# Kernel tuning notes

Hardware: AMD Instinct MI355X
Metric: run time of the kernel (lower is better)

## Reference

```python
import jax, jax.numpy as jnp
import numpy as np

B, T, C, H, M = 2, 2048, 1024, 16, 64
EPS = 1e-5


def _ln(x, g, b):
    mu = jnp.mean(x, axis=-1, keepdims=True)
    var = jnp.mean(jnp.square(x - mu), axis=-1, keepdims=True)
    return (x - mu) * jax.lax.rsqrt(var + EPS) * g + b


def setup_inputs() -> dict:
    key = jax.random.key(0)
    ks = jax.random.split(key, 16)
    s = lambda fan_in: 1.0 / np.sqrt(fan_in)
    return {
        'x': jax.random.normal(ks[0], (B, T, C), jnp.float32),
        'ln1_g': jnp.ones((C,), jnp.float32),
        'ln1_b': jnp.zeros((C,), jnp.float32),
        'attn_w': jax.random.normal(ks[1], (C, 3 * C), jnp.float32) * s(C),
        'attn_b': jnp.zeros((3 * C,), jnp.float32),
        'proj_w': jax.random.normal(ks[2], (C, C), jnp.float32) * s(C),
        'proj_b': jnp.zeros((C,), jnp.float32),
        'a1_dw': jax.random.normal(ks[3], (C, M), jnp.float32) * s(C),
        'a1_db': jnp.zeros((M,), jnp.float32),
        'a1_uw': jax.random.normal(ks[4], (M, C), jnp.float32) * s(M),
        'a1_ub': jnp.zeros((C,), jnp.float32),
        'ln2_g': jnp.ones((C,), jnp.float32),
        'ln2_b': jnp.zeros((C,), jnp.float32),
        'fc_w': jax.random.normal(ks[5], (C, 4 * C), jnp.float32) * s(C),
        'fc_b': jnp.zeros((4 * C,), jnp.float32),
        'mlp_pw': jax.random.normal(ks[6], (4 * C, C), jnp.float32) * s(4 * C),
        'mlp_pb': jnp.zeros((C,), jnp.float32),
        'a2_dw': jax.random.normal(ks[7], (C, M), jnp.float32) * s(C),
        'a2_db': jnp.zeros((M,), jnp.float32),
        'a2_uw': jax.random.normal(ks[8], (M, C), jnp.float32) * s(M),
        'a2_ub': jnp.zeros((C,), jnp.float32),
    }


def _attn(x, attn_w, attn_b, proj_w, proj_b):
    b, t, c = x.shape
    hd = c // H
    qkv = x @ attn_w + attn_b                      # [B,T,3C]
    q, k, v = jnp.split(qkv, 3, axis=-1)
    q = q.reshape(b, t, H, hd).transpose(0, 2, 1, 3)  # [B,H,T,hd]
    k = k.reshape(b, t, H, hd).transpose(0, 2, 1, 3)
    v = v.reshape(b, t, H, hd).transpose(0, 2, 1, 3)
    att = jnp.einsum('bhqd,bhkd->bhqk', q, k) * (1.0 / np.sqrt(hd))
    mask = jnp.tril(jnp.ones((t, t), bool))
    att = jnp.where(mask, att, -jnp.inf)
    att = jax.nn.softmax(att, axis=-1)
    y = jnp.einsum('bhqk,bhkd->bhqd', att, v)      # [B,H,T,hd]
    y = y.transpose(0, 2, 1, 3).reshape(b, t, c)
    return y @ proj_w + proj_b


def _adapter(x, dw, db, uw, ub):
    return jax.nn.relu(x @ dw + db) @ uw + ub


def reference(x, ln1_g, ln1_b, attn_w, attn_b, proj_w, proj_b,
              a1_dw, a1_db, a1_uw, a1_ub, ln2_g, ln2_b,
              fc_w, fc_b, mlp_pw, mlp_pb, a2_dw, a2_db, a2_uw, a2_ub):
    x = x + _attn(_ln(x, ln1_g, ln1_b), attn_w, attn_b, proj_w, proj_b)
    x = x + _adapter(x, a1_dw, a1_db, a1_uw, a1_ub)
    h = _ln(x, ln2_g, ln2_b)
    h = jax.nn.gelu(h @ fc_w + fc_b, approximate=True) @ mlp_pw + mlp_pb
    x = x + h
    x = x + _adapter(x, a2_dw, a2_db, a2_uw, a2_ub)
    return x
```

## Files before the change

kernel.cpp:

```cpp
#include <hip/hip_runtime.h>
#include <hip/hip_bf16.h>
#include <cstdint>

#define DEVI __device__ __forceinline__

using bf16x8 = __attribute__((ext_vector_type(8))) short;
using f32x4  = __attribute__((ext_vector_type(4))) float;

DEVI short f2b(float f) {
  __hip_bfloat16 h = __float2bfloat16(f);
  return *reinterpret_cast<short*>(&h);
}
DEVI float b2f(short s) {
  __hip_bfloat16 h = *reinterpret_cast<__hip_bfloat16*>(&s);
  return __bfloat162float(h);
}
DEVI uint32_t pk2(float a, float b) {
  return (uint32_t)(uint16_t)f2b(a) | ((uint32_t)(uint16_t)f2b(b) << 16);
}

DEVI f32x4 mfma16(bf16x8 a, bf16x8 b, f32x4 c) {
  return __builtin_amdgcn_mfma_f32_16x16x32_bf16(a, b, c, 0, 0, 0);
}

DEVI void gload_lds16(const void* g, void* l) {
  __builtin_amdgcn_global_load_lds(
      (const __attribute__((address_space(1))) void*)g,
      (__attribute__((address_space(3))) void*)l, 16, 0, 0);
}

DEVI float gelu_f(float x) {
  float u = 1.5957691216057308f * (x + 0.044715f * x * x * x);
  float e = __expf(u);
  float t = 1.f - 2.f / (e + 1.f);
  return 0.5f * x * (1.f + t);
}

__global__ void k_wt(const float* __restrict__ in, short* __restrict__ out,
                     int R, int Cc) {
  __shared__ float tile[32][33];
  int c0 = blockIdx.x * 32;
  int r0 = blockIdx.y * 32;
  int tx = threadIdx.x, ty = threadIdx.y;
  for (int i = ty; i < 32; i += 8) {
    int r = r0 + i, c = c0 + tx;
    tile[i][tx] = (r < R && c < Cc) ? in[(size_t)r * Cc + c] : 0.f;
  }
  __syncthreads();
  for (int i = ty; i < 32; i += 8) {
    int orow = c0 + i;
    int ocol = r0 + tx;
    if (orow < Cc && ocol < R) out[(size_t)orow * R + ocol] = f2b(tile[tx][i]);
  }
}

__global__ void k_layernorm(const float* __restrict__ x, const float* __restrict__ g,
                            const float* __restrict__ bta, short* __restrict__ out) {
  const int C = 1024;
  int row = blockIdx.x;
  const float* xr = x + (size_t)row * C;
  f32x4 v = *(const f32x4*)(xr + threadIdx.x * 4);
  float s = v[0] + v[1] + v[2] + v[3];
  float s2 = v[0]*v[0] + v[1]*v[1] + v[2]*v[2] + v[3]*v[3];
#pragma unroll
  for (int m = 1; m < 64; m <<= 1) { s += __shfl_xor(s, m); s2 += __shfl_xor(s2, m); }
  __shared__ float red[8];
  int w = threadIdx.x >> 6;
  if ((threadIdx.x & 63) == 0) { red[w] = s; red[4 + w] = s2; }
  __syncthreads();
  s = red[0] + red[1] + red[2] + red[3];
  s2 = red[4] + red[5] + red[6] + red[7];
  float mu = s * (1.f / 1024.f);
  float rstd = rsqrtf(s2 * (1.f / 1024.f) - mu * mu + 1e-5f);
#pragma unroll
  for (int j = 0; j < 4; ++j) {
    int c = threadIdx.x * 4 + j;
    out[(size_t)row * C + c] = f2b((v[j] - mu) * rstd * g[c] + bta[c]);
  }
}

__global__ void k_vtrans(const short* __restrict__ qkv, short* __restrict__ vT) {
  __shared__ short tile[32][72];
  int b = blockIdx.z, h = blockIdx.y;
  int t0 = blockIdx.x * 32;
  int tx = threadIdx.x;
  int ty = threadIdx.y;
  const size_t inbase = ((size_t)(b * 2048 + t0)) * 3072 + 2048 + h * 64;
  for (int i = ty; i < 32; i += 8) {
    tile[i][tx]      = qkv[inbase + (size_t)i * 3072 + tx];
    tile[i][tx + 32] = qkv[inbase + (size_t)i * 3072 + tx + 32];
  }
  __syncthreads();
  const size_t outbase = ((size_t)(b * 16 + h) * 64) * 2048 + t0;
  for (int d = ty; d < 64; d += 8)
    vT[outbase + (size_t)d * 2048 + tx] = tile[tx][d];
}

template <int BM, int BN, int WGM, int WGN, int ACT, bool RESID, bool OUTF, bool OUTB>
__global__ __launch_bounds__(256, 2) void k_gemm(
    const short* __restrict__ A, const short* __restrict__ BT,
    const float* __restrict__ bias, const float* __restrict__ resid,
    float* __restrict__ outf, short* __restrict__ outb,
    int M, int N, int K) {
  static_assert(WGM * WGN == 4, "4 waves");
  constexpr int TM = BM / WGM, TN = BN / WGN;
  constexpr int FM = TM / 16, FN = TN / 16;
  __shared__ short As[BM * 32];
  __shared__ short Bs[BN * 32];
  const int tid = threadIdx.x;
  const int wid = tid >> 6, l = tid & 63, lr = l & 15, lg = l >> 4;
  const int wm = wid / WGN, wn = wid % WGN;
  const int rowA0 = blockIdx.x * BM;
  const int colB0 = blockIdx.y * BN;

  f32x4 acc[FM][FN];
#pragma unroll
  for (int i = 0; i < FM; ++i)
#pragma unroll
    for (int j = 0; j < FN; ++j) acc[i][j] = f32x4{0.f, 0.f, 0.f, 0.f};

  for (int k0 = 0; k0 < K; k0 += 32) {
    __syncthreads();
#pragma unroll
    for (int it = 0; it < (BM * 64) / 4096; ++it) {
      int bo = it * 4096 + tid * 16;
      int row = bo >> 6, col = (bo & 63) >> 1;
      gload_lds16(A + (size_t)(rowA0 + row) * K + k0 + col, (void*)(As + (bo >> 1)));
    }
#pragma unroll
    for (int it = 0; it < (BN * 64) / 4096; ++it) {
      int bo = it * 4096 + tid * 16;
      int row = bo >> 6, col = (bo & 63) >> 1;
      gload_lds16(BT + (size_t)(colB0 + row) * K + k0 + col, (void*)(Bs + (bo >> 1)));
    }
    __syncthreads();
    bf16x8 af[FM], bfr[FN];
#pragma unroll
    for (int i = 0; i < FM; ++i)
      af[i] = *(const bf16x8*)(As + (wm * TM + i * 16 + lr) * 32 + lg * 8);
#pragma unroll
    for (int j = 0; j < FN; ++j)
      bfr[j] = *(const bf16x8*)(Bs + (wn * TN + j * 16 + lr) * 32 + lg * 8);
#pragma unroll
    for (int i = 0; i < FM; ++i)
#pragma unroll
      for (int j = 0; j < FN; ++j)
        acc[i][j] = mfma16(af[i], bfr[j], acc[i][j]);
  }

  const int row0 = rowA0 + wm * TM + lg * 4;
  const int col0 = colB0 + wn * TN + lr;
#pragma unroll
  for (int i = 0; i < FM; ++i) {
#pragma unroll
    for (int j = 0; j < FN; ++j) {
#pragma unroll
      for (int r = 0; r < 4; ++r) {
        int row = row0 + i * 16 + r;
        int col = col0 + j * 16;
        float v = acc[i][j][r] + bias[col];
        if (ACT == 1) v = fmaxf(v, 0.f);
        if (ACT == 2) v = gelu_f(v);
        size_t idx = (size_t)row * N + col;
        if (RESID) v += resid[idx];
        if (OUTF) outf[idx] = v;
        if (OUTB) outb[idx] = f2b(v);
      }
    }
  }
}

__global__ __launch_bounds__(256, 3) void k_attn(
    const short* __restrict__ qkv, const short* __restrict__ vT,
    short* __restrict__ y) {
  constexpr int T = 2048, C3 = 3072;
  const int tid = threadIdx.x;
  const int wid = tid >> 6, l = tid & 63, lr = l & 15, lg = l >> 4;
  const int bh = blockIdx.x, b = bh >> 4, h = bh & 15;
  const int qt = (int)(gridDim.y - 1 - blockIdx.y);
  const int q0 = qt * 64 + wid * 16;

  const float qscale = 0.125f * 1.4426950408889634f;
  const short* qptr = qkv + (size_t)(b * T + q0 + lr) * C3 + h * 64;
  bf16x8 qr0 = *(const bf16x8*)(qptr + lg * 8);
  bf16x8 qr1 = *(const bf16x8*)(qptr + 32 + lg * 8);
  bf16x8 qf0, qf1;
#pragma unroll
  for (int j = 0; j < 8; ++j) {
    qf0[j] = f2b(b2f(qr0[j]) * qscale);
    qf1[j] = f2b(b2f(qr1[j]) * qscale);
  }

  const short* kbase = qkv + (size_t)(b * T) * C3 + 1024 + h * 64;
  const short* vtb = vT + (size_t)bh * 64 * 2048;

  f32x4 o[4];
#pragma unroll
  for (int d = 0; d < 4; ++d) o[d] = f32x4{0.f, 0.f, 0.f, 0.f};
  float m = -1e30f, lsum = 0.f;

  const bool lglt2 = (lg < 2);
  const bool lg0 = (lg == 0), lg1 = (lg == 1), lg2 = (lg == 2), lg3 = (lg == 3);
  const int q = q0 + lr;

  auto loadK = [&](bf16x8* kf, int kv0) {
    const short* kp = kbase + (size_t)(kv0 + lr) * C3;
    kf[0] = *(const bf16x8*)(kp + lg * 8);
    kf[1] = *(const bf16x8*)(kp + 32 + lg * 8);
    kf[2] = *(const bf16x8*)(kp + 16 * C3 + lg * 8);
    kf[3] = *(const bf16x8*)(kp + 16 * C3 + 32 + lg * 8);
  };

  auto tile = [&](bf16x8* kf, bf16x8* knext, int kv0, bool pre) {
    bf16x8 vf0 = *(const bf16x8*)(vtb + (size_t)(0 * 16 + lr) * 2048 + kv0 + lg * 8);
    bf16x8 vf1 = *(const bf16x8*)(vtb + (size_t)(1 * 16 + lr) * 2048 + kv0 + lg * 8);
    bf16x8 vf2 = *(const bf16x8*)(vtb + (size_t)(2 * 16 + lr) * 2048 + kv0 + lg * 8);
    bf16x8 vf3 = *(const bf16x8*)(vtb + (size_t)(3 * 16 + lr) * 2048 + kv0 + lg * 8);
    if (pre) loadK(knext, kv0 + 32);

    f32x4 s0 = {0.f, 0.f, 0.f, 0.f}, s1 = {0.f, 0.f, 0.f, 0.f};
    s0 = mfma16(kf[0], qf0, s0);
    s0 = mfma16(kf[1], qf1, s0);
    s1 = mfma16(kf[2], qf0, s1);
    s1 = mfma16(kf[3], qf1, s1);

#pragma unroll
    for (int r = 0; r < 4; ++r) {
      if (kv0 + lg * 4 + r > q) s0[r] = -1e30f;
      if (kv0 + 16 + lg * 4 + r > q) s1[r] = -1e30f;
    }

    float mx = fmaxf(fmaxf(fmaxf(s0[0], s0[1]), fmaxf(s0[2], s0[3])),
                     fmaxf(fmaxf(s1[0], s1[1]), fmaxf(s1[2], s1[3])));
    mx = fmaxf(mx, __shfl_xor(mx, 16));
    mx = fmaxf(mx, __shfl_xor(mx, 32));
    if (__any(mx > m + 8.f)) {
      float mn = fmaxf(m, mx);
      float corr = exp2f(m - mn);
      m = mn;
      lsum *= corr;
#pragma unroll
      for (int d = 0; d < 4; ++d)
#pragma unroll
        for (int r = 0; r < 4; ++r) o[d][r] *= corr;
    }
    float p0 = exp2f(s0[0] - m), p1 = exp2f(s0[1] - m);
    float p2 = exp2f(s0[2] - m), p3 = exp2f(s0[3] - m);
    float p4 = exp2f(s1[0] - m), p5 = exp2f(s1[1] - m);
    float p6 = exp2f(s1[2] - m), p7 = exp2f(s1[3] - m);
    lsum += ((p0 + p1) + (p2 + p3)) + ((p4 + p5) + (p6 + p7));

    uint32_t a0 = pk2(p0, p1), a1 = pk2(p2, p3);
    uint32_t b0 = pk2(p4, p5), b1 = pk2(p6, p7);
    uint32_t ux = lglt2 ? b0 : a0;
    uint32_t uy = lglt2 ? b1 : a1;
    uint32_t rx0 = (uint32_t)__shfl_xor((int)ux, 32);
    uint32_t rx1 = (uint32_t)__shfl_xor((int)uy, 32);
    uint32_t vx = lg1 ? a0 : (lg2 ? b0 : rx0);
    uint32_t vy = lg1 ? a1 : (lg2 ? b1 : rx1);
    uint32_t rv0 = (uint32_t)__shfl_xor((int)vx, 16);
    uint32_t rv1 = (uint32_t)__shfl_xor((int)vy, 16);
    union {
      bf16x8 v;
      uint32_t u[4];
    } P;
    P.u[0] = lg0 ? a0 : (lg2 ? rx0 : rv0);
    P.u[1] = lg0 ? a1 : (lg2 ? rx1 : rv1);
    P.u[2] = lg3 ? b0 : (lg1 ? rx0 : rv0);
    P.u[3] = lg3 ? b1 : (lg1 ? rx1 : rv1);

    o[0] = mfma16(vf0, P.v, o[0]);
    o[1] = mfma16(vf1, P.v, o[1]);
    o[2] = mfma16(vf2, P.v, o[2]);
    o[3] = mfma16(vf3, P.v, o[3]);
  };

  bf16x8 KA[4], KB[4];
  loadK(KA, 0);
  const int n = (q0 >> 5) + 1;
  int t = 0, kv0 = 0;
  while (true) {
    tile(KA, KB, kv0, t + 1 < n);
    ++t; kv0 += 32;
    if (t == n) break;
    tile(KB, KA, kv0, t + 1 < n);
    ++t; kv0 += 32;
    if (t == n) break;
  }

  lsum += __shfl_xor(lsum, 16);
  lsum += __shfl_xor(lsum, 32);
  float inv = 1.f / lsum;

  short* yp = y + (size_t)(b * T + q0 + lr) * 1024 + h * 64;
#pragma unroll
  for (int dt = 0; dt < 4; ++dt) {
    uint2 wv;
    wv.x = pk2(o[dt][0] * inv, o[dt][1] * inv);
    wv.y = pk2(o[dt][2] * inv, o[dt][3] * inv);
    *(uint2*)(yp + dt * 16 + lg * 4) = wv;
  }
}

extern "C" void kernel_launch(void* const* d_in, const int* in_sizes, int n_in,
                              void* d_out, int out_size, void* d_ws, size_t ws_size,
                              hipStream_t stream) {
  (void)in_sizes; (void)n_in; (void)out_size; (void)ws_size;
  const float* x0     = (const float*)d_in[0];
  const float* ln1_g  = (const float*)d_in[1];
  const float* ln1_b  = (const float*)d_in[2];
  const float* attn_w = (const float*)d_in[3];
  const float* attn_b = (const float*)d_in[4];
  const float* proj_w = (const float*)d_in[5];
  const float* proj_b = (const float*)d_in[6];
  const float* a1_dw  = (const float*)d_in[7];
  const float* a1_db  = (const float*)d_in[8];
  const float* a1_uw  = (const float*)d_in[9];
  const float* a1_ub  = (const float*)d_in[10];
  const float* ln2_g  = (const float*)d_in[11];
  const float* ln2_b  = (const float*)d_in[12];
  const float* fc_w   = (const float*)d_in[13];
  const float* fc_b   = (const float*)d_in[14];
  const float* mlp_pw = (const float*)d_in[15];
  const float* mlp_pb = (const float*)d_in[16];
  const float* a2_dw  = (const float*)d_in[17];
  const float* a2_db  = (const float*)d_in[18];
  const float* a2_uw  = (const float*)d_in[19];
  const float* a2_ub  = (const float*)d_in[20];

  char* ws = (char*)d_ws;
  size_t off = 0;
  auto alloc = [&](size_t bytes) {
    char* p = ws + off;
    off = (off + bytes + 255) & ~(size_t)255;
    return p;
  };

  short* attn_wT = (short*)alloc(3072ull * 1024 * 2);
  short* proj_wT = (short*)alloc(1024ull * 1024 * 2);
  short* fc_wT   = (short*)alloc(4096ull * 1024 * 2);
  short* mlp_pwT = (short*)alloc(1024ull * 4096 * 2);
  short* a1_dwT  = (short*)alloc(64ull * 1024 * 2);
  short* a1_uwT  = (short*)alloc(1024ull * 64 * 2);
  short* a2_dwT  = (short*)alloc(64ull * 1024 * 2);
  short* a2_uwT  = (short*)alloc(1024ull * 64 * 2);
  short* lnb     = (short*)alloc(4096ull * 1024 * 2);
  char*  big     = alloc(4096ull * 4096 * 2);
  short* qkvb    = (short*)big;
  short* vTb     = (short*)(big + 4096ull * 3072 * 2);
  short* fcb     = (short*)big;
  short* yb      = (short*)alloc(4096ull * 1024 * 2);
  float* x1f     = (float*)alloc(4096ull * 1024 * 4);
  float* x2f     = (float*)alloc(4096ull * 1024 * 4);
  short* x1b     = (short*)alloc(4096ull * 1024 * 2);
  short* hb      = (short*)alloc(4096ull * 64 * 2);

  dim3 tb(32, 8);
  k_wt<<<dim3(3072 / 32, 1024 / 32), tb, 0, stream>>>(attn_w, attn_wT, 1024, 3072);
  k_wt<<<dim3(1024 / 32, 1024 / 32), tb, 0, stream>>>(proj_w, proj_wT, 1024, 1024);
  k_wt<<<dim3(4096 / 32, 1024 / 32), tb, 0, stream>>>(fc_w, fc_wT, 1024, 4096);
  k_wt<<<dim3(1024 / 32, 4096 / 32), tb, 0, stream>>>(mlp_pw, mlp_pwT, 4096, 1024);
  k_wt<<<dim3(64 / 32, 1024 / 32), tb, 0, stream>>>(a1_dw, a1_dwT, 1024, 64);
  k_wt<<<dim3(1024 / 32, 64 / 32), tb, 0, stream>>>(a1_uw, a1_uwT, 64, 1024);
  k_wt<<<dim3(64 / 32, 1024 / 32), tb, 0, stream>>>(a2_dw, a2_dwT, 1024, 64);
  k_wt<<<dim3(1024 / 32, 64 / 32), tb, 0, stream>>>(a2_uw, a2_uwT, 64, 1024);

  k_layernorm<<<4096, 256, 0, stream>>>(x0, ln1_g, ln1_b, lnb);

  k_gemm<128, 128, 2, 2, 0, false, false, true><<<dim3(32, 24), 256, 0, stream>>>(
      lnb, attn_wT, attn_b, nullptr, nullptr, qkvb, 4096, 3072, 1024);

  k_vtrans<<<dim3(64, 16, 2), tb, 0, stream>>>(qkvb, vTb);

  k_attn<<<dim3(32, 32), 256, 0, stream>>>(qkvb, vTb, yb);

  k_gemm<128, 128, 2, 2, 0, true, true, true><<<dim3(32, 8), 256, 0, stream>>>(
      yb, proj_wT, proj_b, x0, x1f, x1b, 4096, 1024, 1024);

  k_gemm<64, 64, 2, 2, 1, false, false, true><<<dim3(64, 1), 256, 0, stream>>>(
      x1b, a1_dwT, a1_db, nullptr, nullptr, hb, 4096, 64, 1024);

  k_gemm<128, 128, 2, 2, 0, true, true, false><<<dim3(32, 8), 256, 0, stream>>>(
      hb, a1_uwT, a1_ub, x1f, x2f, nullptr, 4096, 1024, 64);

  k_layernorm<<<4096, 256, 0, stream>>>(x2f, ln2_g, ln2_b, lnb);

  k_gemm<128, 128, 2, 2, 2, false, false, true><<<dim3(32, 32), 256, 0, stream>>>(
      lnb, fc_wT, fc_b, nullptr, nullptr, fcb, 4096, 4096, 1024);

  k_gemm<128, 128, 2, 2, 0, true, true, true><<<dim3(32, 8), 256, 0, stream>>>(
      fcb, mlp_pwT, mlp_pb, x2f, x1f, x1b, 4096, 1024, 4096);

  k_gemm<64, 64, 2, 2, 1, false, false, true><<<dim3(64, 1), 256, 0, stream>>>(
      x1b, a2_dwT, a2_db, nullptr, nullptr, hb, 4096, 64, 1024);

  k_gemm<128, 128, 2, 2, 0, true, true, false><<<dim3(32, 8), 256, 0, stream>>>(
      hb, a2_uwT, a2_ub, x1f, (float*)d_out, nullptr, 4096, 1024, 64);
}
```

Before: 551.6 us.

## Stage K/V tiles through double-buffered LDS shared by eight attention waves

The attention kernel now uses 512-thread blocks covering 128 queries. Each K and V^T tile of 32 keys is loaded once per block into swizzled, double-buffered LDS with direct global-to-LDS loads, instead of each wave loading K and V straight from global memory into registers. The aim is to cut redundant global/L2 traffic and overlap the next tile's load with the current tile's compute. In exchange, every tile now needs a block-wide barrier, and waves whose queries lie before the current tile sit idle at those barriers under the causal mask.

```diff
diff --git a/kernel.cpp b/kernel.cpp
--- a/kernel.cpp
+++ b/kernel.cpp
@@ -170,7 +170,7 @@
   }
 }
 
-__global__ __launch_bounds__(256, 3) void k_attn(
+__global__ __launch_bounds__(512, 4) void k_attn(
     const short* __restrict__ qkv, const short* __restrict__ vT,
     short* __restrict__ y) {
   constexpr int T = 2048, C3 = 3072;
@@ -178,7 +178,9 @@
   const int wid = tid >> 6, l = tid & 63, lr = l & 15, lg = l >> 4;
   const int bh = blockIdx.x, b = bh >> 4, h = bh & 15;
   const int qt = (int)(gridDim.y - 1 - blockIdx.y);
-  const int q0 = qt * 64 + wid * 16;
+  const int q0 = qt * 128 + wid * 16;
+
+  __shared__ short lds[2][4096];
 
   const float qscale = 0.125f * 1.4426950408889634f;
   const short* qptr = qkv + (size_t)(b * T + q0 + lr) * C3 + h * 64;
@@ -194,6 +196,28 @@
   const short* kbase = qkv + (size_t)(b * T) * C3 + 1024 + h * 64;
   const short* vtb = vT + (size_t)bh * 64 * 2048;
 
+  const bool isK = (tid < 256);
+  const int p = (isK ? tid : (tid - 256)) * 16;
+  int sK_row = 0, sK_half = 0, sV_d = 0, sV_half = 0;
+  {
+    if (isK) {
+      int s = p ^ (((p >> 7) & 7) << 4);
+      sK_row = s >> 7; sK_half = (s & 127) >> 1;
+    } else {
+      int s = p ^ (((p >> 7) & 3) << 4);
+      sV_d = s >> 6; sV_half = (s & 63) >> 1;
+    }
+  }
+  short* dst0 = &lds[0][(isK ? 0 : 2048) + (p >> 1)];
+  short* dst1 = &lds[1][(isK ? 0 : 2048) + (p >> 1)];
+
+  auto STAGE = [&](int buf, int kv0) {
+    const short* g = isK
+        ? kbase + (size_t)(kv0 + sK_row) * C3 + sK_half
+        : vtb + (size_t)sV_d * T + kv0 + sV_half;
+    gload_lds16(g, buf ? dst1 : dst0);
+  };
+
   f32x4 o[4];
 #pragma unroll
   for (int d = 0; d < 4; ++d) o[d] = f32x4{0.f, 0.f, 0.f, 0.f};
@@ -202,27 +226,30 @@
   const bool lglt2 = (lg < 2);
   const bool lg0 = (lg == 0), lg1 = (lg == 1), lg2 = (lg == 2), lg3 = (lg == 3);
   const int q = q0 + lr;
-
-  auto loadK = [&](bf16x8* kf, int kv0) {
-    const short* kp = kbase + (size_t)(kv0 + lr) * C3;
-    kf[0] = *(const bf16x8*)(kp + lg * 8);
-    kf[1] = *(const bf16x8*)(kp + 32 + lg * 8);
-    kf[2] = *(const bf16x8*)(kp + 16 * C3 + lg * 8);
-    kf[3] = *(const bf16x8*)(kp + 16 * C3 + 32 + lg * 8);
-  };
-
-  auto tile = [&](bf16x8* kf, bf16x8* knext, int kv0, bool pre) {
-    bf16x8 vf0 = *(const bf16x8*)(vtb + (size_t)(0 * 16 + lr) * 2048 + kv0 + lg * 8);
-    bf16x8 vf1 = *(const bf16x8*)(vtb + (size_t)(1 * 16 + lr) * 2048 + kv0 + lg * 8);
-    bf16x8 vf2 = *(const bf16x8*)(vtb + (size_t)(2 * 16 + lr) * 2048 + kv0 + lg * 8);
-    bf16x8 vf3 = *(const bf16x8*)(vtb + (size_t)(3 * 16 + lr) * 2048 + kv0 + lg * 8);
-    if (pre) loadK(knext, kv0 + 32);
+  const int xk = (lr & 7) << 4;
+  const int ck0 = (lg * 16) ^ xk;
+  const int ck1 = (64 + lg * 16) ^ xk;
+
+  auto compute = [&](int buf, int kv0) {
+    const short* Kl = &lds[buf][0];
+    const short* Vl = &lds[buf][2048];
+    bf16x8 kf0 = *(const bf16x8*)(Kl + ((lr * 128 + ck0) >> 1));
+    bf16x8 kf1 = *(const bf16x8*)(Kl + ((lr * 128 + ck1) >> 1));
+    bf16x8 kf2 = *(const bf16x8*)(Kl + (((16 + lr) * 128 + ck0) >> 1));
+    bf16x8 kf3 = *(const bf16x8*)(Kl + (((16 + lr) * 128 + ck1) >> 1));
+    bf16x8 vf[4];
+#pragma unroll
+    for (int dt = 0; dt < 4; ++dt) {
+      int row = dt * 16 + lr;
+      int cv = (lg * 16) ^ (((row >> 1) & 3) << 4);
+      vf[dt] = *(const bf16x8*)(Vl + ((row * 64 + cv) >> 1));
+    }
 
     f32x4 s0 = {0.f, 0.f, 0.f, 0.f}, s1 = {0.f, 0.f, 0.f, 0.f};
-    s0 = mfma16(kf[0], qf0, s0);
-    s0 = mfma16(kf[1], qf1, s0);
-    s1 = mfma16(kf[2], qf0, s1);
-    s1 = mfma16(kf[3], qf1, s1);
+    s0 = mfma16(kf0, qf0, s0);
+    s0 = mfma16(kf1, qf1, s0);
+    s1 = mfma16(kf2, qf0, s1);
+    s1 = mfma16(kf3, qf1, s1);
 
 #pragma unroll
     for (int r = 0; r < 4; ++r) {
@@ -269,23 +296,22 @@
     P.u[2] = lg3 ? b0 : (lg1 ? rx0 : rv0);
     P.u[3] = lg3 ? b1 : (lg1 ? rx1 : rv1);
 
-    o[0] = mfma16(vf0, P.v, o[0]);
-    o[1] = mfma16(vf1, P.v, o[1]);
-    o[2] = mfma16(vf2, P.v, o[2]);
-    o[3] = mfma16(vf3, P.v, o[3]);
+    o[0] = mfma16(vf[0], P.v, o[0]);
+    o[1] = mfma16(vf[1], P.v, o[1]);
+    o[2] = mfma16(vf[2], P.v, o[2]);
+    o[3] = mfma16(vf[3], P.v, o[3]);
   };
 
-  bf16x8 KA[4], KB[4];
-  loadK(KA, 0);
-  const int n = (q0 >> 5) + 1;
-  int t = 0, kv0 = 0;
-  while (true) {
-    tile(KA, KB, kv0, t + 1 < n);
-    ++t; kv0 += 32;
-    if (t == n) break;
-    tile(KB, KA, kv0, t + 1 < n);
-    ++t; kv0 += 32;
-    if (t == n) break;
+  const int ntb = 4 * (qt + 1);
+  const int myend = q0 + 15;
+  STAGE(0, 0);
+  __syncthreads();
+  int cur = 0, kv0 = 0;
+  for (int t = 0; t < ntb; ++t, kv0 += 32) {
+    if (t + 1 < ntb) STAGE(cur ^ 1, kv0 + 32);
+    if (kv0 <= myend) compute(cur, kv0);
+    __syncthreads();
+    cur ^= 1;
   }
 
   lsum += __shfl_xor(lsum, 16);
@@ -372,7 +398,7 @@
 
   k_vtrans<<<dim3(64, 16, 2), tb, 0, stream>>>(qkvb, vTb);
 
-  k_attn<<<dim3(32, 32), 256, 0, stream>>>(qkvb, vTb, yb);
+  k_attn<<<dim3(32, 16), 512, 0, stream>>>(qkvb, vTb, yb);
 
   k_gemm<128, 128, 2, 2, 0, true, true, true><<<dim3(32, 8), 256, 0, stream>>>(
       yb, proj_wT, proj_b, x0, x1f, x1b, 4096, 1024, 1024);
```

Result: faster. 480.0 us (-13.0%).
